# Performance work log

Hardware: AMD Instinct MI355X
Metric: run time of the kernel (lower is better)

## Reference

```python
import jax, jax.numpy as jnp
import numpy as np

R = 16            # search_range
D = 2 * R + 1     # 33 offsets per axis -> 1089 cost channels
B, C, H, W = 64, 256, 16, 16
OUT = 512         # conv channels for search_range=16
FULLY = 1024
EPS_BN = 1e-5
EPS_NORM = 1e-12
LRELU_SLOPE = 0.01


def l2_normalize(x):
    # torch F.normalize(x, dim=1, p=2): x / clamp_min(||x||_2, 1e-12)
    n = jnp.sqrt(jnp.sum(x * x, axis=1, keepdims=True))
    return x / jnp.maximum(n, EPS_NORM)


def cost_volume(c1, warp, r):
    # Fused equivalent of the original (2r+1)^2 Python-loop of slice/mul/mean:
    # one dense correlation GEMM over the padded map, then a gather of the
    # diagonal-band entries. cost[b,dy,dx,i,j] = mean_c c1[b,c,i,j]*pad[b,c,i+dy,j+dx]
    b, c, h, w = c1.shape
    d = 2 * r + 1
    padded = jnp.pad(warp, ((0, 0), (0, 0), (r, r), (r, r)))          # (B,C,h+2r,w+2r)
    full = jnp.einsum('bcij,bcuv->bijuv', c1, padded) / c             # (B,h,w,h+2r,w+2r)
    dy = jnp.arange(d)
    ii = jnp.arange(h)
    jj = jnp.arange(w)
    I = ii[None, None, :, None]                 # (1,1,h,1)
    J = jj[None, None, None, :]                 # (1,1,1,w)
    U = dy[:, None, None, None] + I             # (d,1,h,1)
    V = dy[None, :, None, None] + J             # (1,d,1,w)
    cost = full[:, I, J, U, V]                  # (B,d,d,h,w)
    cost = cost.reshape(b, d * d, h, w)
    return jnp.where(cost > 0, cost, LRELU_SLOPE * cost)  # LeakyReLU(0.01)


def conv_bn_relu(x, Wc, bc, g, be, stride):
    y = jax.lax.conv_general_dilated(
        x, Wc, window_strides=(stride, stride), padding=((1, 1), (1, 1)),
        dimension_numbers=('NCHW', 'OIHW', 'NCHW'))
    y = y + bc[None, :, None, None]
    # training-mode BatchNorm: biased batch stats over (B,H,W)
    mu = jnp.mean(y, axis=(0, 2, 3), keepdims=True)
    var = jnp.var(y, axis=(0, 2, 3), keepdims=True)
    y = (y - mu) * jax.lax.rsqrt(var + EPS_BN)
    y = y * g[None, :, None, None] + be[None, :, None, None]
    return jnp.maximum(y, 0.0)


def setup_inputs() -> dict:
    key = jax.random.key(0)
    ks = jax.random.split(key, 10)
    s = 0.02
    inp = {
        'feature1': jax.random.normal(ks[0], (B, C, H, W), jnp.float32),
        'feature2': jax.random.normal(ks[1], (B, C, H, W), jnp.float32),
        'W1': jax.random.normal(ks[2], (OUT, D * D, 3, 3), jnp.float32) * s,
        'b1': jnp.zeros((OUT,), jnp.float32),
        'g1': jnp.ones((OUT,), jnp.float32),
        'be1': jnp.zeros((OUT,), jnp.float32),
        'W2': jax.random.normal(ks[3], (OUT, OUT, 3, 3), jnp.float32) * s,
        'b2': jnp.zeros((OUT,), jnp.float32),
        'g2': jnp.ones((OUT,), jnp.float32),
        'be2': jnp.zeros((OUT,), jnp.float32),
        'W3': jax.random.normal(ks[4], (OUT, OUT, 3, 3), jnp.float32) * s,
        'b3': jnp.zeros((OUT,), jnp.float32),
        'g3': jnp.ones((OUT,), jnp.float32),
        'be3': jnp.zeros((OUT,), jnp.float32),
        'Wf1': jax.random.normal(ks[5], (FULLY, 256 * OUT), jnp.float32) * s,
        'bf1': jnp.zeros((FULLY,), jnp.float32),
        'Wf2': jax.random.normal(ks[6], (8, FULLY), jnp.float32) * s,
        'bf2': jnp.zeros((8,), jnp.float32),
    }
    return inp


def reference(feature1, feature2, W1, b1, g1, be1, W2, b2, g2, be2,
              W3, b3, g3, be3, Wf1, bf1, Wf2, bf2):
    # warped=False: normalize both feature maps
    gc = cost_volume(l2_normalize(feature1), l2_normalize(feature2), R)
    x = conv_bn_relu(gc, W1, b1, g1, be1, 1)
    x = conv_bn_relu(x, W2, b2, g2, be2, 1)
    x = conv_bn_relu(x, W3, b3, g3, be3, 1)
    x = x.reshape(x.shape[0], -1)               # (B, 512*16*16)
    x = jnp.maximum(x @ Wf1.T + bf1, 0.0)       # Linear + ReLU
    # Dropout treated as identity (deterministic reference)
    offset = x @ Wf2.T + bf2                    # (B, 8)
    return offset
```

## Files before the change

kernel.cpp:

```cpp
#include <hip/hip_runtime.h>
#include <hip/hip_bf16.h>
#include <stdint.h>


typedef unsigned short ushort_t;
typedef __attribute__((ext_vector_type(8))) short     bf16x8;
typedef __attribute__((ext_vector_type(8))) unsigned short u16x8;
typedef __attribute__((ext_vector_type(4))) unsigned short u16x4;
typedef __attribute__((ext_vector_type(2))) unsigned short u16x2;
typedef __attribute__((ext_vector_type(4))) float     f32x4;

#define NB   64
#define NC   256
#define NP   256
#define KP1  1152
#define NOUT 512
#define NROWS 16384
#define KFC  131072
#define NF   1024
#define KSPL 32

__device__ __forceinline__ unsigned short f2bf(float x) {
  union { float f; unsigned u; } c; c.f = x;
  unsigned r = c.u + 0x7FFFu + ((c.u >> 16) & 1u);
  return (unsigned short)(r >> 16);
}
__device__ __forceinline__ float b2f(unsigned short u) {
  union { unsigned u; float f; } c; c.u = ((unsigned)u) << 16; return c.f;
}

__device__ __forceinline__ void gl_lds16(const void* g, void* l) {
  __builtin_amdgcn_global_load_lds(
      (const __attribute__((address_space(1))) unsigned int*)g,
      (__attribute__((address_space(3))) unsigned int*)l, 16, 0, 0);
}

__device__ __forceinline__ f32x4 mfma16(bf16x8 a, bf16x8 b, f32x4 c) {
  return __builtin_amdgcn_mfma_f32_16x16x32_bf16(a, b, c, 0, 0, 0);
}

__global__ __launch_bounds__(1024) void l2norm_t(
    const float* __restrict__ f1, const float* __restrict__ f2,
    ushort_t* __restrict__ AT, ushort_t* __restrict__ N2T)
{
  __shared__ float red[4][256];
  const float* src = blockIdx.y ? f2 : f1;
  ushort_t*    dst = blockIdx.y ? N2T : AT;
  const int b = blockIdx.x;
  const int pos = threadIdx.x & 255, q = threadIdx.x >> 8;
  const float* sb = src + (size_t)b * NC * NP;
  float sq = 0.f;
  for (int c = q * 64; c < q * 64 + 64; ++c) {
    float v = sb[c * NP + pos]; sq += v * v;
  }
  red[q][pos] = sq;
  __syncthreads();
  float tot = red[0][pos] + red[1][pos] + red[2][pos] + red[3][pos];
  float sc = 1.f / fmaxf(sqrtf(tot), 1e-12f);
  ushort_t* db = dst + ((size_t)b * NP + pos) * NC;
#pragma unroll
  for (int j = 0; j < 8; ++j) {
    int c0 = q * 64 + j * 8;
    u16x8 pk;
#pragma unroll
    for (int k = 0; k < 8; ++k) pk[k] = f2bf(sb[(c0 + k) * NP + pos] * sc);
    *(u16x8*)(db + c0) = pk;
  }
}

#define T1P (9 * NOUT * KP1)
#define T23 (9 * NOUT * 512)
__global__ __launch_bounds__(256) void pack_all(
    const float* __restrict__ W1, const float* __restrict__ W2,
    const float* __restrict__ W3, ushort_t* __restrict__ Wp1,
    ushort_t* __restrict__ Wp2, ushort_t* __restrict__ Wp3)
{
  int p = blockIdx.x * 256 + threadIdx.x;
  const float* W; ushort_t* Wp; int Cin, Kp, q;
  if (p < T1P)            { W = W1; Wp = Wp1; Cin = 1089; Kp = KP1; q = p; }
  else if (p < T1P + T23) { W = W2; Wp = Wp2; Cin = 512;  Kp = 512; q = p - T1P; }
  else if (p < T1P + 2 * T23) { W = W3; Wp = Wp3; Cin = 512; Kp = 512; q = p - T1P - T23; }
  else return;
  int tap = q / (NOUT * Kp);
  int rem = q - tap * (NOUT * Kp);
  int o   = rem / Kp;
  int cin = rem - o * Kp;
  float v = (cin < Cin) ? W[((size_t)o * Cin + cin) * 9 + tap] : 0.f;
  Wp[q] = f2bf(v);
}

__global__ __launch_bounds__(256) void corr_gemm(
    const ushort_t* __restrict__ AT,
    const ushort_t* __restrict__ N2T,
    float* __restrict__ C)
{
  __shared__ ushort_t As[128 * 64];
  __shared__ ushort_t Bs[128 * 64];
  const int tid = threadIdx.x, lane = tid & 63, wave = tid >> 6;
  const int wr = wave >> 1, wc = wave & 1;
  const int la = lane & 15, lb = lane >> 4;
  const int b  = blockIdx.z;
  const int m0 = blockIdx.y * 128;
  const int n0 = blockIdx.x * 128;

  f32x4 acc[4][4];
#pragma unroll
  for (int i = 0; i < 4; ++i)
#pragma unroll
    for (int j = 0; j < 4; ++j) acc[i][j] = (f32x4){0.f, 0.f, 0.f, 0.f};

  const ushort_t* srcA[4];
  const ushort_t* srcB[4];
#pragma unroll
  for (int s = 0; s < 4; ++s) {
    int idx = tid + (s << 8);
    int row = idx >> 3, c16 = idx & 7;
    srcA[s] = AT  + ((size_t)b * NP + m0 + row) * NC + c16 * 8;
    srcB[s] = N2T + ((size_t)b * NP + n0 + row) * NC + c16 * 8;
  }

  for (int kc = 0; kc < NC; kc += 64) {
#pragma unroll
    for (int s = 0; s < 4; ++s) {
      int idx = tid + (s << 8);
      gl_lds16(srcA[s] + kc, &As[idx * 8]);
      gl_lds16(srcB[s] + kc, &Bs[idx * 8]);
    }
    __syncthreads();
#pragma unroll
    for (int kk = 0; kk < 2; ++kk) {
      bf16x8 af[4], bfv[4];
#pragma unroll
      for (int mi = 0; mi < 4; ++mi)
        af[mi] = *(const bf16x8*)&As[(wr * 64 + mi * 16 + la) * 64 + kk * 32 + lb * 8];
#pragma unroll
      for (int ni = 0; ni < 4; ++ni)
        bfv[ni] = *(const bf16x8*)&Bs[(wc * 64 + ni * 16 + la) * 64 + kk * 32 + lb * 8];
#pragma unroll
      for (int mi = 0; mi < 4; ++mi)
#pragma unroll
        for (int ni = 0; ni < 4; ++ni)
          acc[mi][ni] = mfma16(af[mi], bfv[ni], acc[mi][ni]);
    }
    __syncthreads();
  }

#pragma unroll
  for (int ni = 0; ni < 4; ++ni) {
    int col = n0 + wc * 64 + ni * 16 + la;
#pragma unroll
    for (int mi = 0; mi < 4; ++mi) {
      int p = m0 + wr * 64 + mi * 16 + lb * 4;
#pragma unroll
      for (int r = 0; r < 4; ++r)
        C[((size_t)b * NP + p + r) * NP + col] = acc[mi][ni][r];
    }
  }
}

__global__ __launch_bounds__(576) void cost_write(
    const float* __restrict__ C, ushort_t* __restrict__ costT)
{
  __shared__ float row[256];
  const int ij = blockIdx.x, b = blockIdx.y, tid = threadIdx.x;
  const float* cr = C + ((size_t)b * NP + ij) * NP;
  if (tid < 256) row[tid] = cr[tid];
  __syncthreads();
  const int i = ij >> 4, j = ij & 15;
  const int d0 = tid * 2;
  u16x2 pk;
#pragma unroll
  for (int q = 0; q < 2; ++q) {
    int dd = d0 + q;
    int dy = dd / 33;
    int dx = dd - dy * 33;
    int oi = dy + i - 16, oj = dx + j - 16;
    float v = 0.f;
    if (((unsigned)oi < 16u) & ((unsigned)oj < 16u))
      v = row[oi * 16 + oj] * (1.f / 256.f);
    v = v > 0.f ? v : 0.01f * v;
    pk[q] = f2bf(v);
  }
  *(u16x2*)(costT + ((size_t)b * NP + ij) * KP1 + d0) = pk;
}

__global__ __launch_bounds__(512, 1) void conv_fused(
    const ushort_t* __restrict__ X, const ushort_t* __restrict__ Wp,
    const float* __restrict__ bias, ushort_t* __restrict__ Y,
    float* __restrict__ st, const int K, const int TPT, const int NT,
    const ushort_t* __restrict__ zerot)
{
  __shared__ ushort_t lds[2 * 24576];
  const int tid = threadIdx.x;
  const int lane = tid & 63, wave = tid >> 6;
  const int wr = wave >> 2, wc = wave & 3;
  const int la = lane & 15, lb = lane >> 4;

  const int bid = blockIdx.x;
  const int L = ((bid & 7) << 5) + (bid >> 3);
  const int b = L >> 2;
  const int n0 = (L & 3) << 7;

  int amask[4];
  const ushort_t* abase[4];
  const ushort_t* bbase[2];
#pragma unroll
  for (int s = 0; s < 4; ++s) {
    int idx = tid + (s << 9);
    int ks = idx & 7, loc = (idx >> 3) & 63;
    int rA = ((s & 1) << 7) + ((s >> 1) << 6) + loc;
    int i = rA >> 4, j = rA & 15;
    int m = 0;
#pragma unroll
    for (int tap = 0; tap < 9; ++tap) {
      int i2 = i + tap / 3 - 1, j2 = j + tap % 3 - 1;
      if (((unsigned)i2 < 16u) & ((unsigned)j2 < 16u)) m |= 1 << tap;
    }
    amask[s] = m;
    abase[s] = X + (size_t)(b * NP + rA) * K + ((ks ^ (rA & 7)) << 3);
  }
#pragma unroll
  for (int s = 0; s < 2; ++s) {
    int idx = tid + (s << 9);
    int ks = idx & 7, loc = (idx >> 3) & 63;
    int rB = (s << 6) + loc;
    bbase[s] = Wp + (size_t)(n0 + rB) * K + ((ks ^ (rB & 7)) << 3);
  }

  const int ck0 = ((0 + lb) ^ (la & 7)) << 3;
  const int ck1 = ((4 + lb) ^ (la & 7)) << 3;
  const int a_base = wr * 4096 + la * 64;
  const int b_off  = 16384 + (wc * 32 + la) * 64;

  f32x4 acc[8][2];
#pragma unroll
  for (int i = 0; i < 8; ++i)
#pragma unroll
    for (int j = 0; j < 2; ++j) acc[i][j] = (f32x4){0.f, 0.f, 0.f, 0.f};

  auto tile_par = [&](int tg, int& toffA, size_t& wtap, int& tap) {
    tap = tg / TPT;
    int kc = (tg - tap * TPT) << 6;
    int ty = tap / 3;
    toffA = (ty * 16 + (tap - 3 * ty) - 17) * K + kc;
    wtap  = (size_t)tap * NOUT * K + kc;
  };

#define FSTAGE_A(S) { const ushort_t* gp = ((amask[S] >> tapN) & 1) ? abase[S] + toffN : zerot; \
                      gl_lds16(gp, &bufn[(tid + ((S) << 9)) * 8]); }
#define FSTAGE_B(S) gl_lds16(bbase[S] + wtapN, &bufn[16384 + (tid + ((S) << 9)) * 8]);
#define FREAD_A03() \
  Af[0][0] = *(const bf16x8*)&buf[a_base + 0    + ck0]; Af[0][1] = *(const bf16x8*)&buf[a_base + 0    + ck1]; \
  Af[1][0] = *(const bf16x8*)&buf[a_base + 1024 + ck0]; Af[1][1] = *(const bf16x8*)&buf[a_base + 1024 + ck1]; \
  Af[2][0] = *(const bf16x8*)&buf[a_base + 2048 + ck0]; Af[2][1] = *(const bf16x8*)&buf[a_base + 2048 + ck1]; \
  Af[3][0] = *(const bf16x8*)&buf[a_base + 3072 + ck0]; Af[3][1] = *(const bf16x8*)&buf[a_base + 3072 + ck1];
#define FREAD_A47() \
  Af[0][0] = *(const bf16x8*)&buf[a_base + 8192 + 0    + ck0]; Af[0][1] = *(const bf16x8*)&buf[a_base + 8192 + 0    + ck1]; \
  Af[1][0] = *(const bf16x8*)&buf[a_base + 8192 + 1024 + ck0]; Af[1][1] = *(const bf16x8*)&buf[a_base + 8192 + 1024 + ck1]; \
  Af[2][0] = *(const bf16x8*)&buf[a_base + 8192 + 2048 + ck0]; Af[2][1] = *(const bf16x8*)&buf[a_base + 8192 + 2048 + ck1]; \
  Af[3][0] = *(const bf16x8*)&buf[a_base + 8192 + 3072 + ck0]; Af[3][1] = *(const bf16x8*)&buf[a_base + 8192 + 3072 + ck1];
#define FREAD_B() \
  Bf[0][0] = *(const bf16x8*)&buf[b_off + 0    + ck0]; Bf[0][1] = *(const bf16x8*)&buf[b_off + 0    + ck1]; \
  Bf[1][0] = *(const bf16x8*)&buf[b_off + 1024 + ck0]; Bf[1][1] = *(const bf16x8*)&buf[b_off + 1024 + ck1];
#define FMFMA(AB) \
  acc[(AB)+0][0] = mfma16(Af[0][0], Bf[0][0], acc[(AB)+0][0]); \
  acc[(AB)+0][1] = mfma16(Af[0][0], Bf[1][0], acc[(AB)+0][1]); \
  acc[(AB)+1][0] = mfma16(Af[1][0], Bf[0][0], acc[(AB)+1][0]); \
  acc[(AB)+1][1] = mfma16(Af[1][0], Bf[1][0], acc[(AB)+1][1]); \
  acc[(AB)+2][0] = mfma16(Af[2][0], Bf[0][0], acc[(AB)+2][0]); \
  acc[(AB)+2][1] = mfma16(Af[2][0], Bf[1][0], acc[(AB)+2][1]); \
  acc[(AB)+3][0] = mfma16(Af[3][0], Bf[0][0], acc[(AB)+3][0]); \
  acc[(AB)+3][1] = mfma16(Af[3][0], Bf[1][0], acc[(AB)+3][1]); \
  acc[(AB)+0][0] = mfma16(Af[0][1], Bf[0][1], acc[(AB)+0][0]); \
  acc[(AB)+0][1] = mfma16(Af[0][1], Bf[1][1], acc[(AB)+0][1]); \
  acc[(AB)+1][0] = mfma16(Af[1][1], Bf[0][1], acc[(AB)+1][0]); \
  acc[(AB)+1][1] = mfma16(Af[1][1], Bf[1][1], acc[(AB)+1][1]); \
  acc[(AB)+2][0] = mfma16(Af[2][1], Bf[0][1], acc[(AB)+2][0]); \
  acc[(AB)+2][1] = mfma16(Af[2][1], Bf[1][1], acc[(AB)+2][1]); \
  acc[(AB)+3][0] = mfma16(Af[3][1], Bf[0][1], acc[(AB)+3][0]); \
  acc[(AB)+3][1] = mfma16(Af[3][1], Bf[1][1], acc[(AB)+3][1]);

  {
    ushort_t* bufn = &lds[0];
    int tapN, toffN; size_t wtapN;
    tile_par(0, toffN, wtapN, tapN);
    FSTAGE_A(0) FSTAGE_A(1) FSTAGE_B(0) FSTAGE_B(1) FSTAGE_A(2) FSTAGE_A(3)
  }
  asm volatile("s_waitcnt vmcnt(2)" ::: "memory");
  __builtin_amdgcn_s_barrier();

  for (int t = 0; t < NT - 1; ++t) {
    const ushort_t* buf = &lds[(t & 1) * 24576];
    ushort_t* bufn = &lds[((t + 1) & 1) * 24576];
    int tapN, toffN; size_t wtapN;
    tile_par(t + 1, toffN, wtapN, tapN);
    bf16x8 Af[4][2], Bf[2][2];

    FREAD_A03()
    FREAD_B()
    FSTAGE_A(0) FSTAGE_A(1) FSTAGE_B(0) FSTAGE_B(1)
    asm volatile("s_waitcnt vmcnt(4)" ::: "memory");
    __builtin_amdgcn_s_barrier();
    asm volatile("s_waitcnt lgkmcnt(0)" ::: "memory");
    __builtin_amdgcn_sched_barrier(0);
    __builtin_amdgcn_s_setprio(1);
    FMFMA(0)
    __builtin_amdgcn_s_setprio(0);

    FREAD_A47()
    FSTAGE_A(2) FSTAGE_A(3)
    asm volatile("s_waitcnt vmcnt(2)" ::: "memory");
    __builtin_amdgcn_s_barrier();
    asm volatile("s_waitcnt lgkmcnt(0)" ::: "memory");
    __builtin_amdgcn_sched_barrier(0);
    __builtin_amdgcn_s_setprio(1);
    FMFMA(4)
    __builtin_amdgcn_s_setprio(0);
  }

  {
    const ushort_t* buf = &lds[((NT - 1) & 1) * 24576];
    bf16x8 Af[4][2], Bf[2][2];
    FREAD_A03()
    FREAD_B()
    asm volatile("s_waitcnt vmcnt(0)" ::: "memory");
    __builtin_amdgcn_s_barrier();
    asm volatile("s_waitcnt lgkmcnt(0)" ::: "memory");
    __builtin_amdgcn_sched_barrier(0);
    FMFMA(0)
    FREAD_A47()
    asm volatile("s_waitcnt lgkmcnt(0)" ::: "memory");
    __builtin_amdgcn_sched_barrier(0);
    FMFMA(4)
  }

#pragma unroll
  for (int ni = 0; ni < 2; ++ni) {
    int col = n0 + wc * 32 + ni * 16 + la;
    float bv = bias[col];
    float s = 0.f, qq = 0.f;
#pragma unroll
    for (int mi = 0; mi < 8; ++mi) {
      int row = b * NP + wr * 128 + mi * 16 + lb * 4;
#pragma unroll
      for (int r = 0; r < 4; ++r) {
        float v = acc[mi][ni][r] + bv;
        Y[(size_t)(row + r) * NOUT + col] = f2bf(v);
        s += v; qq += v * v;
      }
    }
    s  += __shfl_xor(s, 16);  s  += __shfl_xor(s, 32);
    qq += __shfl_xor(qq, 16); qq += __shfl_xor(qq, 32);
    if (lb == 0) {
      atomicAdd(&st[col], s);
      atomicAdd(&st[512 + col], qq);
    }
  }
#undef FSTAGE_A
#undef FSTAGE_B
#undef FREAD_A03
#undef FREAD_A47
#undef FREAD_B
#undef FMFMA
}

__global__ __launch_bounds__(256) void bn_apply_s(
    const ushort_t* __restrict__ Y, const float* __restrict__ st,
    const float* __restrict__ g, const float* __restrict__ be,
    ushort_t* __restrict__ Xo)
{
  const size_t idx = (size_t)blockIdx.x * 256 + threadIdx.x;
  u16x8 a = *(const u16x8*)(Y + idx * 8);
  const int c0 = (int)((idx * 8) & 511);
  u16x8 pk;
#pragma unroll
  for (int q = 0; q < 8; ++q) {
    int cc = c0 + q;
    float y = b2f(a[q]);
    float mu  = st[cc] * (1.f / 16384.f);
    float var = st[512 + cc] * (1.f / 16384.f) - mu * mu;
    float s = rsqrtf(var + 1e-5f) * g[cc];
    pk[q] = f2bf(fmaxf((y - mu) * s + be[cc], 0.f));
  }
  *(u16x8*)(Xo + idx * 8) = pk;
}

__global__ __launch_bounds__(256) void bn_apply_ts(
    const ushort_t* __restrict__ Y, const float* __restrict__ st,
    const float* __restrict__ g, const float* __restrict__ be,
    ushort_t* __restrict__ Xf)
{
  __shared__ ushort_t T[64][65];
  const int c0  = blockIdx.x * 64;
  const int ij0 = blockIdx.y * 64;
  const int b   = blockIdx.z;
  const int tid = threadIdx.x;

#pragma unroll
  for (int it = 0; it < 16; ++it) {
    int e = it * 256 + tid;
    int ij = e >> 6, c = e & 63;
    int cg = c0 + c;
    float y = b2f(Y[((size_t)(b * NP + ij0 + ij)) * NOUT + cg]);
    float mu  = st[cg] * (1.f / 16384.f);
    float var = st[512 + cg] * (1.f / 16384.f) - mu * mu;
    float s = rsqrtf(var + 1e-5f) * g[cg];
    T[ij][c] = f2bf(fmaxf((y - mu) * s + be[cg], 0.f));
  }
  __syncthreads();
#pragma unroll
  for (int it = 0; it < 16; ++it) {
    int e = it * 256 + tid;
    int cr = e >> 6, ijc = e & 63;
    Xf[(size_t)b * KFC + (size_t)(c0 + cr) * NP + ij0 + ijc] = T[ijc][cr];
  }
}

__device__ __forceinline__ u16x8 pack8(float4 a, float4 b) {
  u16x8 r;
  r[0] = f2bf(a.x); r[1] = f2bf(a.y); r[2] = f2bf(a.z); r[3] = f2bf(a.w);
  r[4] = f2bf(b.x); r[5] = f2bf(b.y); r[6] = f2bf(b.z); r[7] = f2bf(b.w);
  return r;
}

__global__ __launch_bounds__(256) void fc1_gemm(
    const ushort_t* __restrict__ Xf, const float* __restrict__ Wf1,
    float* __restrict__ hacc)
{
  __shared__ ushort_t As[64 * 64];
  __shared__ ushort_t Bs[64 * 64];
  const int tid = threadIdx.x, lane = tid & 63, wave = tid >> 6;
  const int la = lane & 15, lb = lane >> 4;
  const int f0 = blockIdx.x * 64;
  const int k0 = blockIdx.y * 4096;

  f32x4 acc[4];
#pragma unroll
  for (int i = 0; i < 4; ++i) acc[i] = (f32x4){0.f, 0.f, 0.f, 0.f};

  const ushort_t* xrow[2];
#pragma unroll
  for (int s = 0; s < 2; ++s) {
    int idx = tid + (s << 8);
    xrow[s] = Xf + (size_t)(idx >> 3) * KFC + k0 + (idx & 7) * 8;
  }
  const int brow = tid >> 2, kseg = (tid & 3) * 16;
  const float* wrow = Wf1 + (size_t)(f0 + brow) * KFC + k0 + kseg;

  for (int kc = 0; kc < 4096; kc += 64) {
#pragma unroll
    for (int s = 0; s < 2; ++s) {
      int idx = tid + (s << 8);
      gl_lds16(xrow[s] + kc, &As[idx * 8]);
    }
    float4 w0 = *(const float4*)(wrow + kc);
    float4 w1 = *(const float4*)(wrow + kc + 4);
    float4 w2 = *(const float4*)(wrow + kc + 8);
    float4 w3 = *(const float4*)(wrow + kc + 12);
    *(u16x8*)&Bs[brow * 64 + kseg]     = pack8(w0, w1);
    *(u16x8*)&Bs[brow * 64 + kseg + 8] = pack8(w2, w3);
    __syncthreads();
#pragma unroll
    for (int kk = 0; kk < 2; ++kk) {
      bf16x8 bfv = *(const bf16x8*)&Bs[(wave * 16 + la) * 64 + kk * 32 + lb * 8];
#pragma unroll
      for (int mi = 0; mi < 4; ++mi) {
        bf16x8 av = *(const bf16x8*)&As[(mi * 16 + la) * 64 + kk * 32 + lb * 8];
        acc[mi] = mfma16(av, bfv, acc[mi]);
      }
    }
    __syncthreads();
  }

  float* slice = hacc + (size_t)blockIdx.y * NB * NF;
#pragma unroll
  for (int mi = 0; mi < 4; ++mi) {
    int row = mi * 16 + lb * 4;
#pragma unroll
    for (int r = 0; r < 4; ++r)
      slice[(size_t)(row + r) * NF + f0 + wave * 16 + la] = acc[mi][r];
  }
}

__global__ __launch_bounds__(256) void fc2_out(
    const float* __restrict__ hacc, const float* __restrict__ bf1,
    const float* __restrict__ Wf2, const float* __restrict__ bf2,
    float* __restrict__ out)
{
  const int b = blockIdx.x, tid = threadIdx.x;
  float a[8];
#pragma unroll
  for (int o = 0; o < 8; ++o) a[o] = 0.f;
  for (int f = tid; f < NF; f += 256) {
    float hv = bf1[f];
#pragma unroll 4
    for (int s = 0; s < KSPL; ++s)
      hv += hacc[((size_t)s * NB + b) * NF + f];
    hv = fmaxf(hv, 0.f);
#pragma unroll
    for (int o = 0; o < 8; ++o) a[o] += hv * Wf2[o * NF + f];
  }
  __shared__ float red[8][256];
#pragma unroll
  for (int o = 0; o < 8; ++o) red[o][tid] = a[o];
  __syncthreads();
  for (int s = 128; s > 0; s >>= 1) {
    if (tid < s) {
#pragma unroll
      for (int o = 0; o < 8; ++o) red[o][tid] += red[o][tid + s];
    }
    __syncthreads();
  }
  if (tid < 8) out[b * 8 + tid] = red[tid][0] + bf2[tid];
}

extern "C" void kernel_launch(void* const* d_in, const int* in_sizes, int n_in,
                              void* d_out, int out_size, void* d_ws, size_t ws_size,
                              hipStream_t stream) {
  const float* f1  = (const float*)d_in[0];
  const float* f2  = (const float*)d_in[1];
  const float* W1  = (const float*)d_in[2];
  const float* b1  = (const float*)d_in[3];
  const float* g1  = (const float*)d_in[4];
  const float* be1 = (const float*)d_in[5];
  const float* W2  = (const float*)d_in[6];
  const float* b2  = (const float*)d_in[7];
  const float* g2  = (const float*)d_in[8];
  const float* be2 = (const float*)d_in[9];
  const float* W3  = (const float*)d_in[10];
  const float* b3  = (const float*)d_in[11];
  const float* g3  = (const float*)d_in[12];
  const float* be3 = (const float*)d_in[13];
  const float* Wf1 = (const float*)d_in[14];
  const float* bf1 = (const float*)d_in[15];
  const float* Wf2 = (const float*)d_in[16];
  const float* bf2 = (const float*)d_in[17];
  float* out = (float*)d_out;

  char* ws = (char*)d_ws;
  size_t off = 0;
  auto alloc = [&](size_t bytes) -> void* {
    void* p = ws + off;
    off += (bytes + 255) & ~(size_t)255;
    return p;
  };

  ushort_t* zerot = (ushort_t*)alloc(256);
  float* st1  = (float*)alloc(1024 * 4);
  float* st2  = (float*)alloc(1024 * 4);
  float* st3  = (float*)alloc(1024 * 4);
  const size_t zero_bytes = off;

  float* hacc = (float*)alloc((size_t)KSPL * NB * NF * 4);
  const size_t SZ_AT   = (size_t)NB * NP * NC * 2;
  const size_t SZ_COST = (size_t)NB * NP * KP1 * 2;
  const size_t SZ_WP1  = (size_t)9 * NOUT * KP1 * 2;
  const size_t SZ_WP23 = (size_t)9 * NOUT * 512 * 2;
  ushort_t* AT    = (ushort_t*)alloc(SZ_AT);
  ushort_t* N2T   = (ushort_t*)alloc(SZ_AT);
  float*    Cbuf  = (float*)alloc((size_t)NB * NP * NP * 4);
  ushort_t* costT = (ushort_t*)alloc(SZ_COST);
  ushort_t* Wp1   = (ushort_t*)alloc(SZ_WP1);
  ushort_t* Wp2   = (ushort_t*)alloc(SZ_WP23);
  ushort_t* Wp3   = (ushort_t*)alloc(SZ_WP23);
  ushort_t* Ybuf  = (ushort_t*)alloc((size_t)NROWS * NOUT * 2);
  ushort_t* Xbuf  = (ushort_t*)alloc((size_t)NROWS * NOUT * 2);
  ushort_t* Xf    = (ushort_t*)alloc((size_t)NB * KFC * 2);

  hipMemsetAsync(ws, 0, zero_bytes, stream);

  l2norm_t<<<dim3(64, 2), 1024, 0, stream>>>(f1, f2, AT, N2T);

  pack_all<<<(T1P + 2 * T23 + 255) / 256, 256, 0, stream>>>(W1, W2, W3, Wp1, Wp2, Wp3);

  corr_gemm<<<dim3(2, 2, 64), 256, 0, stream>>>(AT, N2T, Cbuf);
  cost_write<<<dim3(256, 64), 576, 0, stream>>>(Cbuf, costT);

  conv_fused<<<256, 512, 0, stream>>>(costT, Wp1, b1, Ybuf, st1, KP1, 18, 162, zerot);
  bn_apply_s<<<4096, 256, 0, stream>>>(Ybuf, st1, g1, be1, Xbuf);

  conv_fused<<<256, 512, 0, stream>>>(Xbuf, Wp2, b2, Ybuf, st2, 512, 8, 72, zerot);
  bn_apply_s<<<4096, 256, 0, stream>>>(Ybuf, st2, g2, be2, Xbuf);

  conv_fused<<<256, 512, 0, stream>>>(Xbuf, Wp3, b3, Ybuf, st3, 512, 8, 72, zerot);
  bn_apply_ts<<<dim3(8, 4, 64), 256, 0, stream>>>(Ybuf, st3, g3, be3, Xf);

  fc1_gemm<<<dim3(16, KSPL), 256, 0, stream>>>(Xf, Wf1, hacc);
  fc2_out<<<64, 256, 0, stream>>>(hacc, bf1, Wf2, bf2, out);

  (void)in_sizes; (void)n_in; (void)out_size; (void)ws_size;
}
```

Measured before the change: 569.3 us.

## Double-buffer fc1 GEMM tiles with prefetch and cache l2norm inputs in registers

The fc1 GEMM now uses two LDS buffers for the activation and weight tiles. The next tile's global-to-LDS loads and weight register prefetch are issued while MFMAs run on the current tile, and manual waitcnt plus barriers replace the two syncthreads per iteration. This is meant to hide the memory latency of streaming the large Wf1 matrix. Separately, l2norm_t keeps its 64 loaded values in registers instead of reading the input twice. The hand-placed vmcnt counts are fragile and raise register and LDS use.

Result: no change. 561.0 us (median of 3 runs) (-1.5%).

```diff
diff --git a/kernel.cpp b/kernel.cpp
--- a/kernel.cpp
+++ b/kernel.cpp
@@ -6,7 +6,6 @@
 typedef unsigned short ushort_t;
 typedef __attribute__((ext_vector_type(8))) short     bf16x8;
 typedef __attribute__((ext_vector_type(8))) unsigned short u16x8;
-typedef __attribute__((ext_vector_type(4))) unsigned short u16x4;
 typedef __attribute__((ext_vector_type(2))) unsigned short u16x2;
 typedef __attribute__((ext_vector_type(4))) float     f32x4;
 
@@ -49,10 +48,12 @@
   const int b = blockIdx.x;
   const int pos = threadIdx.x & 255, q = threadIdx.x >> 8;
   const float* sb = src + (size_t)b * NC * NP;
+  float v[64];
+#pragma unroll
+  for (int k = 0; k < 64; ++k) v[k] = sb[(q * 64 + k) * NP + pos];
   float sq = 0.f;
-  for (int c = q * 64; c < q * 64 + 64; ++c) {
-    float v = sb[c * NP + pos]; sq += v * v;
-  }
+#pragma unroll
+  for (int k = 0; k < 64; ++k) sq += v[k] * v[k];
   red[q][pos] = sq;
   __syncthreads();
   float tot = red[0][pos] + red[1][pos] + red[2][pos] + red[3][pos];
@@ -60,11 +61,10 @@
   ushort_t* db = dst + ((size_t)b * NP + pos) * NC;
 #pragma unroll
   for (int j = 0; j < 8; ++j) {
-    int c0 = q * 64 + j * 8;
     u16x8 pk;
 #pragma unroll
-    for (int k = 0; k < 8; ++k) pk[k] = f2bf(sb[(c0 + k) * NP + pos] * sc);
-    *(u16x8*)(db + c0) = pk;
+    for (int k = 0; k < 8; ++k) pk[k] = f2bf(v[j * 8 + k] * sc);
+    *(u16x8*)(db + q * 64 + j * 8) = pk;
   }
 }
 
@@ -427,8 +427,8 @@
     const ushort_t* __restrict__ Xf, const float* __restrict__ Wf1,
     float* __restrict__ hacc)
 {
-  __shared__ ushort_t As[64 * 64];
-  __shared__ ushort_t Bs[64 * 64];
+  __shared__ ushort_t As[2][4096];
+  __shared__ ushort_t Bs[2][4096];
   const int tid = threadIdx.x, lane = tid & 63, wave = tid >> 6;
   const int la = lane & 15, lb = lane >> 4;
   const int f0 = blockIdx.x * 64;
@@ -438,39 +438,72 @@
 #pragma unroll
   for (int i = 0; i < 4; ++i) acc[i] = (f32x4){0.f, 0.f, 0.f, 0.f};
 
-  const ushort_t* xrow[2];
-#pragma unroll
-  for (int s = 0; s < 2; ++s) {
-    int idx = tid + (s << 8);
-    xrow[s] = Xf + (size_t)(idx >> 3) * KFC + k0 + (idx & 7) * 8;
-  }
+  const ushort_t* xrow0 = Xf + (size_t)(tid >> 3) * KFC + k0 + (tid & 7) * 8;
+  const ushort_t* xrow1 = Xf + (size_t)((tid + 256) >> 3) * KFC + k0 + (tid & 7) * 8;
   const int brow = tid >> 2, kseg = (tid & 3) * 16;
   const float* wrow = Wf1 + (size_t)(f0 + brow) * KFC + k0 + kseg;
-
-  for (int kc = 0; kc < 4096; kc += 64) {
-#pragma unroll
-    for (int s = 0; s < 2; ++s) {
-      int idx = tid + (s << 8);
-      gl_lds16(xrow[s] + kc, &As[idx * 8]);
-    }
-    float4 w0 = *(const float4*)(wrow + kc);
-    float4 w1 = *(const float4*)(wrow + kc + 4);
-    float4 w2 = *(const float4*)(wrow + kc + 8);
-    float4 w3 = *(const float4*)(wrow + kc + 12);
-    *(u16x8*)&Bs[brow * 64 + kseg]     = pack8(w0, w1);
-    *(u16x8*)&Bs[brow * 64 + kseg + 8] = pack8(w2, w3);
-    __syncthreads();
-#pragma unroll
-    for (int kk = 0; kk < 2; ++kk) {
-      bf16x8 bfv = *(const bf16x8*)&Bs[(wave * 16 + la) * 64 + kk * 32 + lb * 8];
-#pragma unroll
-      for (int mi = 0; mi < 4; ++mi) {
-        bf16x8 av = *(const bf16x8*)&As[(mi * 16 + la) * 64 + kk * 32 + lb * 8];
-        acc[mi] = mfma16(av, bfv, acc[mi]);
-      }
-    }
-    __syncthreads();
-  }
+  const int bwr = brow * 64 + kseg;
+
+  float4 w0, w1, w2, w3;
+
+  gl_lds16(xrow0, &As[0][tid * 8]);
+  gl_lds16(xrow1, &As[0][(tid + 256) * 8]);
+  w0 = *(const float4*)(wrow + 0);
+  w1 = *(const float4*)(wrow + 4);
+  w2 = *(const float4*)(wrow + 8);
+  w3 = *(const float4*)(wrow + 12);
+  *(u16x8*)&Bs[0][bwr]     = pack8(w0, w1);
+  *(u16x8*)&Bs[0][bwr + 8] = pack8(w2, w3);
+  gl_lds16(xrow0 + 64, &As[1][tid * 8]);
+  gl_lds16(xrow1 + 64, &As[1][(tid + 256) * 8]);
+  w0 = *(const float4*)(wrow + 64);
+  w1 = *(const float4*)(wrow + 68);
+  w2 = *(const float4*)(wrow + 72);
+  w3 = *(const float4*)(wrow + 76);
+  asm volatile("s_waitcnt lgkmcnt(0)" ::: "memory");
+  __builtin_amdgcn_s_barrier();
+
+#define FC1_MFMA(CUR) \
+  { \
+    _Pragma("unroll") \
+    for (int kk = 0; kk < 2; ++kk) { \
+      bf16x8 bfv = *(const bf16x8*)&Bs[CUR][(wave * 16 + la) * 64 + kk * 32 + lb * 8]; \
+      _Pragma("unroll") \
+      for (int mi = 0; mi < 4; ++mi) { \
+        bf16x8 av = *(const bf16x8*)&As[CUR][(mi * 16 + la) * 64 + kk * 32 + lb * 8]; \
+        acc[mi] = mfma16(av, bfv, acc[mi]); \
+      } \
+    } \
+  }
+
+  for (int t = 0; t < 62; ++t) {
+    const int cur = t & 1, nxt = cur ^ 1;
+    FC1_MFMA(cur)
+    *(u16x8*)&Bs[nxt][bwr]     = pack8(w0, w1);
+    *(u16x8*)&Bs[nxt][bwr + 8] = pack8(w2, w3);
+    {
+      const float* wp = wrow + (t + 2) * 64;
+      w0 = *(const float4*)(wp + 0);
+      w1 = *(const float4*)(wp + 4);
+      w2 = *(const float4*)(wp + 8);
+      w3 = *(const float4*)(wp + 12);
+    }
+    asm volatile("s_waitcnt vmcnt(4)" ::: "memory");
+    asm volatile("s_waitcnt lgkmcnt(0)" ::: "memory");
+    __builtin_amdgcn_s_barrier();
+    gl_lds16(xrow0 + (t + 2) * 64, &As[cur][tid * 8]);
+    gl_lds16(xrow1 + (t + 2) * 64, &As[cur][(tid + 256) * 8]);
+  }
+  {
+    FC1_MFMA(0)
+    *(u16x8*)&Bs[1][bwr]     = pack8(w0, w1);
+    *(u16x8*)&Bs[1][bwr + 8] = pack8(w2, w3);
+    asm volatile("s_waitcnt vmcnt(0)" ::: "memory");
+    asm volatile("s_waitcnt lgkmcnt(0)" ::: "memory");
+    __builtin_amdgcn_s_barrier();
+  }
+  FC1_MFMA(1)
+#undef FC1_MFMA
 
   float* slice = hacc + (size_t)blockIdx.y * NB * NF;
 #pragma unroll
```
